# Optimization experiments

Measured on AMD Instinct MI355X. Metric: run time of the kernel, lower is better.

The kernel has to match this reference:

```python
import jax, jax.numpy as jnp
import numpy as np

B, T, C = 2, 2048, 1024
H, D = 16, 64          # n_heads, head_dim
E, K, HD = 8, 2, 1536  # num_experts, active_experts, expert hidden (int(1.5*C))
EPS = 1e-6


def setup_inputs() -> dict:
    key = jax.random.key(0)
    ks = jax.random.split(key, 13)
    s = 0.02
    return {
        "x": jax.random.normal(ks[0], (B, T, C), jnp.float32),
        "rope_cos": jax.random.uniform(ks[1], (T, D), jnp.float32),
        "rope_sin": jax.random.uniform(ks[2], (T, D), jnp.float32),
        "attn_norm_w": jnp.ones((C,), jnp.float32),
        "q_w": jax.random.normal(ks[3], (C, C), jnp.float32) * s,
        "k_w": jax.random.normal(ks[4], (C, C), jnp.float32) * s,
        "v_w": jax.random.normal(ks[5], (C, C), jnp.float32) * s,
        "o_w": jax.random.normal(ks[6], (C, C), jnp.float32) * s,
        "ffn_norm_w": jnp.ones((C,), jnp.float32),
        "router_w": jax.random.normal(ks[7], (E, C), jnp.float32) * s,
        "w1": jax.random.normal(ks[8], (E, HD, C), jnp.float32) * s,
        "w2": jax.random.normal(ks[9], (E, C, HD), jnp.float32) * s,
        "w3": jax.random.normal(ks[10], (E, HD, C), jnp.float32) * s,
    }


def rmsnorm(x, w):
    var = jnp.mean(x * x, axis=-1, keepdims=True)
    return w * x * jax.lax.rsqrt(var + EPS)


def apply_rope(x, cos, sin):
    # x: [B, T, H, D]; cos/sin: [T, D]
    cos = cos[None, :, None, :]
    sin = sin[None, :, None, :]
    d = x.shape[-1] // 2
    x1, x2 = x[..., :d], x[..., d:]
    rotated = jnp.concatenate([-x2, x1], axis=-1)
    return x * cos + rotated * sin


def reference(x, rope_cos, rope_sin, attn_norm_w, q_w, k_w, v_w, o_w,
              ffn_norm_w, router_w, w1, w2, w3):
    b, t, c = x.shape
    h = rmsnorm(x, attn_norm_w)
    q = (h @ q_w.T).reshape(b, t, H, D)
    k = (h @ k_w.T).reshape(b, t, H, D)
    v = (h @ v_w.T).reshape(b, t, H, D)
    q = apply_rope(q, rope_cos[:t], rope_sin[:t]).transpose(0, 2, 1, 3)  # [B,H,T,D]
    k = apply_rope(k, rope_cos[:t], rope_sin[:t]).transpose(0, 2, 1, 3)
    v = v.transpose(0, 2, 1, 3)
    scores = jnp.einsum('bhqd,bhkd->bhqk', q, k) / jnp.sqrt(jnp.asarray(D, q.dtype))
    causal = jnp.tril(jnp.ones((t, t), bool))
    scores = jnp.where(causal, scores, -jnp.inf)
    attn = jax.nn.softmax(scores, axis=-1)
    y = jnp.einsum('bhqk,bhkd->bhqd', attn, v)
    y = y.transpose(0, 2, 1, 3).reshape(b, t, c)
    x = x + y @ o_w.T

    # Sparse MoE (top-K routing, per-expert SwiGLU, weighted combine)
    hn = rmsnorm(x, ffn_norm_w)
    flat = hn.reshape(-1, c)                                # [N, C]
    logits = flat @ router_w.T                              # [N, E]
    wk, idx = jax.lax.top_k(logits, K)                      # [N, K]
    wk = jax.nn.softmax(wk, axis=-1)
    # combined per-expert gate: [N, E] (zero for unrouted experts)
    gate = jnp.sum((idx[..., None] == jnp.arange(E)) * wk[..., None], axis=1)
    out = jnp.zeros_like(flat)
    for e in range(E):
        g = jax.nn.silu(flat @ w1[e].T) * (flat @ w3[e].T)  # [N, HD]
        out = out + gate[:, e:e + 1] * (g @ w2[e].T)
    return x + out.reshape(b, t, c)
```

## Files before the change

### kernel.cpp

```cpp
#include <hip/hip_runtime.h>
#include <hip/hip_bf16.h>
#include <math.h>

#define Bq 2
#define Tq 2048
#define Cq 1024
#define Hq 16
#define Dq 64
#define Eq 8
#define HDq 1536
#define NTOK (Bq*Tq)

typedef unsigned short u16;
typedef unsigned int u32;
typedef _Float16 f16;
typedef __bf16 bf16x8 __attribute__((ext_vector_type(8)));
typedef _Float16 f16x8 __attribute__((ext_vector_type(8)));
typedef float f32x4v __attribute__((ext_vector_type(4)));

#define MB(x) ((size_t)(x) * 262144)

__device__ __forceinline__ float silu_f(float a) {
    return a / (1.0f + __expf(-a));
}
__device__ __forceinline__ u16 f2bf(float f) {
    union { float f; unsigned u; } a; a.f = f;
    unsigned r = a.u + 0x7fffu + ((a.u >> 16) & 1u);
    return (u16)(r >> 16);
}
__device__ __forceinline__ u16 f16bits(f16 h) {
    union { f16 f; u16 u; } a; a.f = h; return a.u;
}

__device__ __forceinline__ void stage16(const void* g, void* l) {
    __builtin_amdgcn_global_load_lds(
        (const __attribute__((address_space(1))) unsigned int*)g,
        (__attribute__((address_space(3))) unsigned int*)l, 16, 0, 0);
}

__global__ __launch_bounds__(256) void rmsnorm_split_k(const float* __restrict__ x,
                                                       const float* __restrict__ w,
                                                       u16* __restrict__ hh,
                                                       u16* __restrict__ hl) {
    int row = blockIdx.x;
    int tid = threadIdx.x;
    const float* xr = x + (size_t)row * Cq;
    float4 v = *(const float4*)(xr + tid * 4);
    float ss = v.x*v.x + v.y*v.y + v.z*v.z + v.w*v.w;
    #pragma unroll
    for (int off = 32; off; off >>= 1) ss += __shfl_xor(ss, off);
    __shared__ float red[4];
    if ((tid & 63) == 0) red[tid >> 6] = ss;
    __syncthreads();
    float tot = red[0] + red[1] + red[2] + red[3];
    float scale = rsqrtf(tot * (1.0f / (float)Cq) + 1e-6f);
    float4 wv = *(const float4*)(w + tid * 4);
    float o[4] = { v.x*wv.x*scale, v.y*wv.y*scale, v.z*wv.z*scale, v.w*wv.w*scale };
    ushort4 oh, ol;
    u16* ph = (u16*)&oh; u16* pl = (u16*)&ol;
    #pragma unroll
    for (int i = 0; i < 4; i++) {
        f16 hi = (f16)o[i]; f16 lo = (f16)(o[i] - (float)hi);
        ph[i] = f16bits(hi); pl[i] = f16bits(lo);
    }
    *(ushort4*)(hh + (size_t)row * Cq + tid * 4) = oh;
    *(ushort4*)(hl + (size_t)row * Cq + tid * 4) = ol;
}

__global__ __launch_bounds__(256) void rmsnorm2_k(const float* __restrict__ x,
                                                  const float* __restrict__ w,
                                                  float* __restrict__ hn,
                                                  u16* __restrict__ hnb) {
    int row = blockIdx.x;
    int tid = threadIdx.x;
    const float* xr = x + (size_t)row * Cq;
    float4 v = *(const float4*)(xr + tid * 4);
    float ss = v.x*v.x + v.y*v.y + v.z*v.z + v.w*v.w;
    #pragma unroll
    for (int off = 32; off; off >>= 1) ss += __shfl_xor(ss, off);
    __shared__ float red[4];
    if ((tid & 63) == 0) red[tid >> 6] = ss;
    __syncthreads();
    float tot = red[0] + red[1] + red[2] + red[3];
    float scale = rsqrtf(tot * (1.0f / (float)Cq) + 1e-6f);
    float4 wv = *(const float4*)(w + tid * 4);
    float4 o = make_float4(v.x*wv.x*scale, v.y*wv.y*scale, v.z*wv.z*scale, v.w*wv.w*scale);
    *(float4*)(hn + (size_t)row * Cq + tid * 4) = o;
    ushort4 ob = make_ushort4(f2bf(o.x), f2bf(o.y), f2bf(o.z), f2bf(o.w));
    *(ushort4*)(hnb + (size_t)row * Cq + tid * 4) = ob;
}

__global__ __launch_bounds__(256) void wconv_k(const float* __restrict__ w1,
                                               const float* __restrict__ w3,
                                               const float* __restrict__ w2,
                                               u16* __restrict__ w1b,
                                               u16* __restrict__ w3b,
                                               u16* __restrict__ w2b) {
    int a = blockIdx.y;
    const float* src = (a == 0) ? w1 : ((a == 1) ? w3 : w2);
    u16* dst = (a == 0) ? w1b : ((a == 1) ? w3b : w2b);
    size_t i = ((size_t)blockIdx.x * 256 + threadIdx.x) * 8;
    float4 f0 = *(const float4*)(src + i);
    float4 f1 = *(const float4*)(src + i + 4);
    ushort4 o0 = make_ushort4(f2bf(f0.x), f2bf(f0.y), f2bf(f0.z), f2bf(f0.w));
    ushort4 o1 = make_ushort4(f2bf(f1.x), f2bf(f1.y), f2bf(f1.z), f2bf(f1.w));
    *(ushort4*)(dst + i)     = o0;
    *(ushort4*)(dst + i + 4) = o1;
}

__global__ __launch_bounds__(256) void wsplit_k(const float* __restrict__ qw,
                                                const float* __restrict__ kw,
                                                const float* __restrict__ vw,
                                                const float* __restrict__ ow,
                                                u16* __restrict__ qhp, u16* __restrict__ qlp,
                                                u16* __restrict__ khp, u16* __restrict__ klp,
                                                u16* __restrict__ vhp, u16* __restrict__ vlp,
                                                u16* __restrict__ ohp, u16* __restrict__ olp) {
    int a = blockIdx.y;
    const float* src = (a == 0) ? qw : ((a == 1) ? kw : ((a == 2) ? vw : ow));
    u16* dh = (a == 0) ? qhp : ((a == 1) ? khp : ((a == 2) ? vhp : ohp));
    u16* dl = (a == 0) ? qlp : ((a == 1) ? klp : ((a == 2) ? vlp : olp));
    size_t i = ((size_t)blockIdx.x * 256 + threadIdx.x) * 8;
    float f[8];
    *(float4*)&f[0] = *(const float4*)(src + i);
    *(float4*)&f[4] = *(const float4*)(src + i + 4);
    u16 oh[8], ol[8];
    #pragma unroll
    for (int j = 0; j < 8; j++) {
        f16 hi = (f16)f[j]; f16 lo = (f16)(f[j] - (float)hi);
        oh[j] = f16bits(hi); ol[j] = f16bits(lo);
    }
    *(uint4*)(dh + i) = *(uint4*)oh;
    *(uint4*)(dl + i) = *(uint4*)ol;
}

__global__ __launch_bounds__(256, 3) void gemm_fused(const u16* __restrict__ Ahg,
                                                     const u16* __restrict__ Alg,
                                                     const float* __restrict__ Wq,
                                                     const float* __restrict__ Wk,
                                                     const float* __restrict__ Wv,
                                                     u16* __restrict__ qh_o,
                                                     u16* __restrict__ ql_o,
                                                     u16* __restrict__ kh_o,
                                                     u16* __restrict__ kl_o,
                                                     float* __restrict__ vf_o,
                                                     const float* __restrict__ cosb,
                                                     const float* __restrict__ sinb,
                                                     const float* __restrict__ aux,
                                                     float* __restrict__ outf,
                                                     int kind) {
    __shared__ u16 AhS[2][128*32], AlS[2][128*32], BhS[128*32], BlS[128*32];
    int tid = threadIdx.x;
    int wave = tid >> 6, lane = tid & 63;
    int wm = wave >> 1, wn = wave & 1;
    int bx = blockIdx.x, by = blockIdx.y;
    int proj, nx;
    const float* W;
    if (kind == 0) {
        proj = bx >> 3; nx = bx & 7;
        W = (proj == 0) ? Wq : ((proj == 1) ? Wk : Wv);
    } else {
        proj = 3; nx = bx; W = Wq;
    }

    int srow = tid >> 2, sch = (tid & 3) * 8;
    const u16* A0 = Ahg + (size_t)(by*128 + srow) * Cq + sch;
    const u16* A1 = A0 + (size_t)64 * Cq;
    const u16* L0 = Alg + (size_t)(by*128 + srow) * Cq + sch;
    const u16* L1 = L0 + (size_t)64 * Cq;
    const float* W0 = W + (size_t)(nx*128 + srow) * Cq + sch;
    const float* W1 = W0 + (size_t)64 * Cq;
    int lo0 = srow*32 + sch, lo1 = lo0 + 2048;

    f32x4v acc[4][4];
    #pragma unroll
    for (int i = 0; i < 4; i++)
        #pragma unroll
        for (int j = 0; j < 4; j++)
            #pragma unroll
            for (int r = 0; r < 4; r++) acc[i][j][r] = 0.0f;

    float wr0[8], wr1[8];
    stage16(A0, &AhS[0][lo0]);
    stage16(A1, &AhS[0][lo1]);
    stage16(L0, &AlS[0][lo0]);
    stage16(L1, &AlS[0][lo1]);
    *(float4*)&wr0[0] = *(const float4*)(W0);
    *(float4*)&wr0[4] = *(const float4*)(W0 + 4);
    *(float4*)&wr1[0] = *(const float4*)(W1);
    *(float4*)&wr1[4] = *(const float4*)(W1 + 4);

    int fr = lane & 15, fk = (lane >> 4) * 8;
    int cur = 0;
    for (int k0 = 0; k0 < Cq; k0 += 32, cur ^= 1) {
        __syncthreads();
        {
            f16x8 bh0, bl0, bh1, bl1;
            #pragma unroll
            for (int i = 0; i < 8; i++) {
                f16 h0 = (f16)wr0[i]; bh0[i] = h0; bl0[i] = (f16)(wr0[i] - (float)h0);
                f16 h1 = (f16)wr1[i]; bh1[i] = h1; bl1[i] = (f16)(wr1[i] - (float)h1);
            }
            *(f16x8*)(void*)&BhS[lo0] = bh0;
            *(f16x8*)(void*)&BlS[lo0] = bl0;
            *(f16x8*)(void*)&BhS[lo1] = bh1;
            *(f16x8*)(void*)&BlS[lo1] = bl1;
        }
        __syncthreads();
        int kn = k0 + 32;
        if (kn < Cq) {
            stage16(A0 + kn, &AhS[cur^1][lo0]);
            stage16(A1 + kn, &AhS[cur^1][lo1]);
            stage16(L0 + kn, &AlS[cur^1][lo0]);
            stage16(L1 + kn, &AlS[cur^1][lo1]);
            *(float4*)&wr0[0] = *(const float4*)(W0 + kn);
            *(float4*)&wr0[4] = *(const float4*)(W0 + kn + 4);
            *(float4*)&wr1[0] = *(const float4*)(W1 + kn);
            *(float4*)&wr1[4] = *(const float4*)(W1 + kn + 4);
        }
        f16x8 ah[4], al[4];
        #pragma unroll
        for (int mi = 0; mi < 4; mi++) {
            ah[mi] = *(const f16x8*)(const void*)&AhS[cur][(wm*64 + mi*16 + fr)*32 + fk];
            al[mi] = *(const f16x8*)(const void*)&AlS[cur][(wm*64 + mi*16 + fr)*32 + fk];
        }
        #pragma unroll
        for (int ni = 0; ni < 4; ni++) {
            f16x8 bhf = *(const f16x8*)(const void*)&BhS[(wn*64 + ni*16 + fr)*32 + fk];
            f16x8 blf = *(const f16x8*)(const void*)&BlS[(wn*64 + ni*16 + fr)*32 + fk];
            #pragma unroll
            for (int mi = 0; mi < 4; mi++) {
                acc[mi][ni] = __builtin_amdgcn_mfma_f32_16x16x32_f16(ah[mi], bhf, acc[mi][ni], 0, 0, 0);
                acc[mi][ni] = __builtin_amdgcn_mfma_f32_16x16x32_f16(ah[mi], blf, acc[mi][ni], 0, 0, 0);
                acc[mi][ni] = __builtin_amdgcn_mfma_f32_16x16x32_f16(al[mi], bhf, acc[mi][ni], 0, 0, 0);
            }
        }
    }

    int cr = (lane >> 4) * 4, cc = lane & 15;
    if (proj < 2) {
        u16* dh = (proj == 0) ? qh_o : kh_o;
        u16* dl = (proj == 0) ? ql_o : kl_o;
        float scale = (proj == 0) ? 0.125f : 1.0f;
        int hd = (nx * 2 + wn) * 64;
        #pragma unroll
        for (int mi = 0; mi < 4; mi++)
            #pragma unroll
            for (int r = 0; r < 4; r++) {
                int row = by*128 + wm*64 + mi*16 + cr + r;
                int t = row & (Tq - 1);
                #pragma unroll
                for (int ni = 0; ni < 2; ni++) {
                    int d0 = ni*16 + cc;
                    float a = acc[mi][ni][r];
                    float b = acc[mi][ni+2][r];
                    float c0 = cosb[t*Dq + d0],      s0 = sinb[t*Dq + d0];
                    float c1 = cosb[t*Dq + d0 + 32], s1 = sinb[t*Dq + d0 + 32];
                    float oa = (a * c0 - b * s0) * scale;
                    float ob = (b * c1 + a * s1) * scale;
                    size_t off = (size_t)row * Cq + hd + d0;
                    f16 ha = (f16)oa;
                    f16 hb = (f16)ob;
                    dh[off]      = f16bits(ha);
                    dl[off]      = f16bits((f16)(oa - (float)ha));
                    dh[off + 32] = f16bits(hb);
                    dl[off + 32] = f16bits((f16)(ob - (float)hb));
                }
            }
    } else if (proj == 2) {
        #pragma unroll
        for (int mi = 0; mi < 4; mi++)
            #pragma unroll
            for (int r = 0; r < 4; r++) {
                int row = by*128 + wm*64 + mi*16 + cr + r;
                #pragma unroll
                for (int ni = 0; ni < 4; ni++)
                    vf_o[(size_t)row * Cq + nx*128 + wn*64 + ni*16 + cc] = acc[mi][ni][r];
            }
    } else {
        #pragma unroll
        for (int mi = 0; mi < 4; mi++)
            #pragma unroll
            for (int r = 0; r < 4; r++) {
                int row = by*128 + wm*64 + mi*16 + cr + r;
                #pragma unroll
                for (int ni = 0; ni < 4; ni++) {
                    size_t off = (size_t)row * Cq + nx*128 + wn*64 + ni*16 + cc;
                    outf[off] = acc[mi][ni][r] + aux[off];
                }
            }
    }
}

__global__ __launch_bounds__(256, 2) void gemm_fused2(const u16* __restrict__ Ahg,
                                                      const u16* __restrict__ Alg,
                                                      const u16* __restrict__ Bh0,
                                                      const u16* __restrict__ Bl0,
                                                      const u16* __restrict__ Bh1,
                                                      const u16* __restrict__ Bl1,
                                                      const u16* __restrict__ Bh2,
                                                      const u16* __restrict__ Bl2,
                                                      u16* __restrict__ qh_o,
                                                      u16* __restrict__ ql_o,
                                                      u16* __restrict__ kh_o,
                                                      u16* __restrict__ kl_o,
                                                      float* __restrict__ vf_o,
                                                      const float* __restrict__ cosb,
                                                      const float* __restrict__ sinb,
                                                      const float* __restrict__ aux,
                                                      float* __restrict__ outf,
                                                      int kind) {
    __shared__ u16 AhS[2][128*32], AlS[2][128*32], BhS[2][128*32], BlS[2][128*32];
    int tid = threadIdx.x;
    int wave = tid >> 6, lane = tid & 63;
    int wm = wave >> 1, wn = wave & 1;
    int bx = blockIdx.x, by = blockIdx.y;
    int proj, nx;
    const u16 *Bh, *Bl;
    if (kind == 0) {
        proj = bx >> 3; nx = bx & 7;
        Bh = (proj == 0) ? Bh0 : ((proj == 1) ? Bh1 : Bh2);
        Bl = (proj == 0) ? Bl0 : ((proj == 1) ? Bl1 : Bl2);
    } else {
        proj = 3; nx = bx; Bh = Bh0; Bl = Bl0;
    }

    int srow = tid >> 2, sch = (tid & 3) * 8;
    const u16* A0 = Ahg + (size_t)(by*128 + srow) * Cq + sch;
    const u16* A1 = A0 + (size_t)64 * Cq;
    const u16* L0 = Alg + (size_t)(by*128 + srow) * Cq + sch;
    const u16* L1 = L0 + (size_t)64 * Cq;
    const u16* H0 = Bh + (size_t)(nx*128 + srow) * Cq + sch;
    const u16* H1 = H0 + (size_t)64 * Cq;
    const u16* G0 = Bl + (size_t)(nx*128 + srow) * Cq + sch;
    const u16* G1 = G0 + (size_t)64 * Cq;
    int lo0 = srow*32 + sch, lo1 = lo0 + 2048;

    f32x4v acc[4][4];
    #pragma unroll
    for (int i = 0; i < 4; i++)
        #pragma unroll
        for (int j = 0; j < 4; j++)
            #pragma unroll
            for (int r = 0; r < 4; r++) acc[i][j][r] = 0.0f;

    stage16(A0, &AhS[0][lo0]); stage16(A1, &AhS[0][lo1]);
    stage16(L0, &AlS[0][lo0]); stage16(L1, &AlS[0][lo1]);
    stage16(H0, &BhS[0][lo0]); stage16(H1, &BhS[0][lo1]);
    stage16(G0, &BlS[0][lo0]); stage16(G1, &BlS[0][lo1]);

    int fr = lane & 15, fk = (lane >> 4) * 8;
    int cur = 0;
    for (int k0 = 0; k0 < Cq; k0 += 32, cur ^= 1) {
        __syncthreads();
        int kn = k0 + 32;
        if (kn < Cq) {
            stage16(A0 + kn, &AhS[cur^1][lo0]); stage16(A1 + kn, &AhS[cur^1][lo1]);
            stage16(L0 + kn, &AlS[cur^1][lo0]); stage16(L1 + kn, &AlS[cur^1][lo1]);
            stage16(H0 + kn, &BhS[cur^1][lo0]); stage16(H1 + kn, &BhS[cur^1][lo1]);
            stage16(G0 + kn, &BlS[cur^1][lo0]); stage16(G1 + kn, &BlS[cur^1][lo1]);
        }
        f16x8 ah[4], al[4];
        #pragma unroll
        for (int mi = 0; mi < 4; mi++) {
            ah[mi] = *(const f16x8*)(const void*)&AhS[cur][(wm*64 + mi*16 + fr)*32 + fk];
            al[mi] = *(const f16x8*)(const void*)&AlS[cur][(wm*64 + mi*16 + fr)*32 + fk];
        }
        #pragma unroll
        for (int ni = 0; ni < 4; ni++) {
            f16x8 bhf = *(const f16x8*)(const void*)&BhS[cur][(wn*64 + ni*16 + fr)*32 + fk];
            f16x8 blf = *(const f16x8*)(const void*)&BlS[cur][(wn*64 + ni*16 + fr)*32 + fk];
            #pragma unroll
            for (int mi = 0; mi < 4; mi++) {
                acc[mi][ni] = __builtin_amdgcn_mfma_f32_16x16x32_f16(ah[mi], bhf, acc[mi][ni], 0, 0, 0);
                acc[mi][ni] = __builtin_amdgcn_mfma_f32_16x16x32_f16(ah[mi], blf, acc[mi][ni], 0, 0, 0);
                acc[mi][ni] = __builtin_amdgcn_mfma_f32_16x16x32_f16(al[mi], bhf, acc[mi][ni], 0, 0, 0);
            }
        }
    }

    int cr = (lane >> 4) * 4, cc = lane & 15;
    if (proj < 2) {
        u16* dh = (proj == 0) ? qh_o : kh_o;
        u16* dl = (proj == 0) ? ql_o : kl_o;
        float scale = (proj == 0) ? 0.125f : 1.0f;
        int hd = (nx * 2 + wn) * 64;
        #pragma unroll
        for (int mi = 0; mi < 4; mi++)
            #pragma unroll
            for (int r = 0; r < 4; r++) {
                int row = by*128 + wm*64 + mi*16 + cr + r;
                int t = row & (Tq - 1);
                #pragma unroll
                for (int ni = 0; ni < 2; ni++) {
                    int d0 = ni*16 + cc;
                    float a = acc[mi][ni][r];
                    float b = acc[mi][ni+2][r];
                    float c0 = cosb[t*Dq + d0],      s0 = sinb[t*Dq + d0];
                    float c1 = cosb[t*Dq + d0 + 32], s1 = sinb[t*Dq + d0 + 32];
                    float oa = (a * c0 - b * s0) * scale;
                    float ob = (b * c1 + a * s1) * scale;
                    size_t off = (size_t)row * Cq + hd + d0;
                    f16 ha = (f16)oa;
                    f16 hb = (f16)ob;
                    dh[off]      = f16bits(ha);
                    dl[off]      = f16bits((f16)(oa - (float)ha));
                    dh[off + 32] = f16bits(hb);
                    dl[off + 32] = f16bits((f16)(ob - (float)hb));
                }
            }
    } else if (proj == 2) {
        #pragma unroll
        for (int mi = 0; mi < 4; mi++)
            #pragma unroll
            for (int r = 0; r < 4; r++) {
                int row = by*128 + wm*64 + mi*16 + cr + r;
                #pragma unroll
                for (int ni = 0; ni < 4; ni++)
                    vf_o[(size_t)row * Cq + nx*128 + wn*64 + ni*16 + cc] = acc[mi][ni][r];
            }
    } else {
        #pragma unroll
        for (int mi = 0; mi < 4; mi++)
            #pragma unroll
            for (int r = 0; r < 4; r++) {
                int row = by*128 + wm*64 + mi*16 + cr + r;
                #pragma unroll
                for (int ni = 0; ni < 4; ni++) {
                    size_t off = (size_t)row * Cq + nx*128 + wn*64 + ni*16 + cc;
                    outf[off] = acc[mi][ni][r] + aux[off];
                }
            }
    }
}

__global__ __launch_bounds__(256) void vtrans_k(const float* __restrict__ v,
                                                u16* __restrict__ vth,
                                                u16* __restrict__ vtl) {
    __shared__ u16 Th[64 * 72];
    __shared__ u16 Tl[64 * 72];
    int tc = blockIdx.x;
    int bh = blockIdx.y;
    int b = bh >> 4, h = bh & 15;
    int tid = threadIdx.x;
    int tr = tid >> 2;
    int dc = (tid & 3) * 16;
    size_t gin = ((size_t)(b * Tq + tc * 64 + tr)) * Cq + h * Dq + dc;
    #pragma unroll
    for (int i = 0; i < 16; i += 4) {
        float4 f = *(const float4*)(v + gin + i);
        float fv[4] = {f.x, f.y, f.z, f.w};
        #pragma unroll
        for (int j = 0; j < 4; j++) {
            f16 hi = (f16)fv[j];
            f16 lo = (f16)(fv[j] - (float)hi);
            Th[(dc + i + j) * 72 + tr] = f16bits(hi);
            Tl[(dc + i + j) * 72 + tr] = f16bits(lo);
        }
    }
    __syncthreads();
    int dr = tid >> 2;
    int cc = (tid & 3) * 16;
    size_t gout = ((size_t)(bh * 64 + dr)) * Tq + tc * 64 + cc;
    *(uint4*)(vth + gout)     = *(uint4*)(Th + dr * 72 + cc);
    *(uint4*)(vth + gout + 8) = *(uint4*)(Th + dr * 72 + cc + 8);
    *(uint4*)(vtl + gout)     = *(uint4*)(Tl + dr * 72 + cc);
    *(uint4*)(vtl + gout + 8) = *(uint4*)(Tl + dr * 72 + cc + 8);
}

#define AST 72
__global__ __launch_bounds__(256, 3) void attn_f16(const u16* __restrict__ qh_g,
                                                   const u16* __restrict__ ql_g,
                                                   const u16* __restrict__ kh_g,
                                                   const u16* __restrict__ kl_g,
                                                   const u16* __restrict__ vth_g,
                                                   const u16* __restrict__ vtl_g,
                                                   u16* __restrict__ yh_g,
                                                   u16* __restrict__ yl_g) {
    __shared__ u16 Kh[64*AST], Kl[64*AST];
    __shared__ u16 Vh[64*AST], Vl[64*AST];

    int id = blockIdx.x;
    int bh = id & 31;
    int qt = 31 - (id >> 5);
    int b = bh >> 4, h = bh & 15;
    int tid = threadIdx.x;
    int wv = tid >> 6, lane = tid & 63;
    int fr = lane & 15, fg = lane >> 4;
    int sr = tid >> 2, sc = (tid & 3) * 16;

    int idx0 = fr + ((fg & 1) << 5);
    int idx1 = idx0 + 16;
    int hiw = fg >> 1;

    uint4 rkh0, rkh1, rkl0, rkl1, rvh0, rvh1, rvl0, rvl1;
    auto ldkv = [&](int kt) {
        size_t kg = ((size_t)(b * Tq + kt * 64 + sr)) * Cq + h * Dq + sc;
        size_t vg = ((size_t)(bh * 64 + sr)) * Tq + kt * 64 + sc;
        rkh0 = *(const uint4*)(kh_g + kg);  rkh1 = *(const uint4*)(kh_g + kg + 8);
        rkl0 = *(const uint4*)(kl_g + kg);  rkl1 = *(const uint4*)(kl_g + kg + 8);
        rvh0 = *(const uint4*)(vth_g + vg); rvh1 = *(const uint4*)(vth_g + vg + 8);
        rvl0 = *(const uint4*)(vtl_g + vg); rvl1 = *(const uint4*)(vtl_g + vg + 8);
    };

    size_t qg = ((size_t)(b * Tq + qt * 64 + wv * 16 + fr)) * Cq + h * Dq + fg * 8;
    f16x8 aqh0 = *(const f16x8*)(const void*)(qh_g + qg);
    f16x8 aqh1 = *(const f16x8*)(const void*)(qh_g + qg + 32);
    f16x8 aql0 = *(const f16x8*)(const void*)(ql_g + qg);
    f16x8 aql1 = *(const f16x8*)(const void*)(ql_g + qg + 32);
    ldkv(0);

    f32x4v acc_o[4];
    float m_i = -1e30f, l_i = 0.0f;
    #pragma unroll
    for (int i = 0; i < 4; i++)
        #pragma unroll
        for (int r = 0; r < 4; r++) acc_o[i][r] = 0.0f;

    for (int kt = 0; kt <= qt; kt++) {
        __syncthreads();
        *(uint4*)(Kh + sr*AST + sc)     = rkh0;
        *(uint4*)(Kh + sr*AST + sc + 8) = rkh1;
        *(uint4*)(Kl + sr*AST + sc)     = rkl0;
        *(uint4*)(Kl + sr*AST + sc + 8) = rkl1;
        *(uint4*)(Vh + sr*AST + sc)     = rvh0;
        *(uint4*)(Vh + sr*AST + sc + 8) = rvh1;
        *(uint4*)(Vl + sr*AST + sc)     = rvl0;
        *(uint4*)(Vl + sr*AST + sc + 8) = rvl1;
        __syncthreads();
        if (kt < qt) ldkv(kt + 1);

        f32x4v s[4];
        __builtin_amdgcn_s_setprio(1);
        #pragma unroll
        for (int ni = 0; ni < 4; ni++) {
            int boff = (ni * 16 + fr) * AST + fg * 8;
            f16x8 kh0 = *(const f16x8*)(const void*)(Kh + boff);
            f16x8 kh1 = *(const f16x8*)(const void*)(Kh + boff + 32);
            f16x8 kl0 = *(const f16x8*)(const void*)(Kl + boff);
            f16x8 kl1 = *(const f16x8*)(const void*)(Kl + boff + 32);
            f32x4v t;
            #pragma unroll
            for (int r = 0; r < 4; r++) t[r] = 0.0f;
            t = __builtin_amdgcn_mfma_f32_16x16x32_f16(kh0, aqh0, t, 0, 0, 0);
            t = __builtin_amdgcn_mfma_f32_16x16x32_f16(kh1, aqh1, t, 0, 0, 0);
            t = __builtin_amdgcn_mfma_f32_16x16x32_f16(kl0, aqh0, t, 0, 0, 0);
            t = __builtin_amdgcn_mfma_f32_16x16x32_f16(kl1, aqh1, t, 0, 0, 0);
            t = __builtin_amdgcn_mfma_f32_16x16x32_f16(kh0, aql0, t, 0, 0, 0);
            t = __builtin_amdgcn_mfma_f32_16x16x32_f16(kh1, aql1, t, 0, 0, 0);
            s[ni] = t;
        }
        __builtin_amdgcn_s_setprio(0);

        if (kt == qt) {
            int qloc = wv * 16 + fr;
            #pragma unroll
            for (int ni = 0; ni < 4; ni++) {
                #pragma unroll
                for (int r = 0; r < 4; r++) {
                    if (ni * 16 + fg * 4 + r > qloc) s[ni][r] = -1e30f;
                }
            }
        }

        float mx = s[0][0];
        #pragma unroll
        for (int ni = 0; ni < 4; ni++)
            #pragma unroll
            for (int r = 0; r < 4; r++) mx = fmaxf(mx, s[ni][r]);
        mx = fmaxf(mx, __shfl_xor(mx, 16));
        mx = fmaxf(mx, __shfl_xor(mx, 32));
        float mn = fmaxf(m_i, mx);
        float p[4][4];
        float rs = 0.0f;
        #pragma unroll
        for (int ni = 0; ni < 4; ni++)
            #pragma unroll
            for (int r = 0; r < 4; r++) {
                p[ni][r] = __expf(s[ni][r] - mn);
                rs += p[ni][r];
            }
        rs += __shfl_xor(rs, 16);
        rs += __shfl_xor(rs, 32);
        float alpha = __expf(m_i - mn);
        l_i = l_i * alpha + rs;
        m_i = mn;

        #pragma unroll
        for (int r = 0; r < 4; r++) {
            float ar = __shfl(alpha, 20 * fg + r);
            #pragma unroll
            for (int ni = 0; ni < 4; ni++) acc_o[ni][r] *= ar;
        }

        u32 wh[8], wl[8];
        #pragma unroll
        for (int ni = 0; ni < 4; ni++) {
            #pragma unroll
            for (int pr = 0; pr < 2; pr++) {
                float pa = p[ni][pr*2], pb = p[ni][pr*2 + 1];
                f16 ha = (f16)pa, hb = (f16)pb;
                wh[ni*2 + pr] = (u32)f16bits(ha) | ((u32)f16bits(hb) << 16);
                f16 la = (f16)(pa - (float)ha), lb = (f16)(pb - (float)hb);
                wl[ni*2 + pr] = (u32)f16bits(la) | ((u32)f16bits(lb) << 16);
            }
        }

        union { u32 u[4]; f16x8 v; } fh0, fh1, fl0, fl1;
        {
            u32 a, c;
            a = __shfl((int)wh[0], idx0); c = __shfl((int)wh[2], idx0);
            fh0.u[0] = hiw ? c : a;
            a = __shfl((int)wh[1], idx0); c = __shfl((int)wh[3], idx0);
            fh0.u[1] = hiw ? c : a;
            a = __shfl((int)wh[0], idx1); c = __shfl((int)wh[2], idx1);
            fh0.u[2] = hiw ? c : a;
            a = __shfl((int)wh[1], idx1); c = __shfl((int)wh[3], idx1);
            fh0.u[3] = hiw ? c : a;
            a = __shfl((int)wh[4], idx0); c = __shfl((int)wh[6], idx0);
            fh1.u[0] = hiw ? c : a;
            a = __shfl((int)wh[5], idx0); c = __shfl((int)wh[7], idx0);
            fh1.u[1] = hiw ? c : a;
            a = __shfl((int)wh[4], idx1); c = __shfl((int)wh[6], idx1);
            fh1.u[2] = hiw ? c : a;
            a = __shfl((int)wh[5], idx1); c = __shfl((int)wh[7], idx1);
            fh1.u[3] = hiw ? c : a;
            a = __shfl((int)wl[0], idx0); c = __shfl((int)wl[2], idx0);
            fl0.u[0] = hiw ? c : a;
            a = __shfl((int)wl[1], idx0); c = __shfl((int)wl[3], idx0);
            fl0.u[1] = hiw ? c : a;
            a = __shfl((int)wl[0], idx1); c = __shfl((int)wl[2], idx1);
            fl0.u[2] = hiw ? c : a;
            a = __shfl((int)wl[1], idx1); c = __shfl((int)wl[3], idx1);
            fl0.u[3] = hiw ? c : a;
            a = __shfl((int)wl[4], idx0); c = __shfl((int)wl[6], idx0);
            fl1.u[0] = hiw ? c : a;
            a = __shfl((int)wl[5], idx0); c = __shfl((int)wl[7], idx0);
            fl1.u[1] = hiw ? c : a;
            a = __shfl((int)wl[4], idx1); c = __shfl((int)wl[6], idx1);
            fl1.u[2] = hiw ? c : a;
            a = __shfl((int)wl[5], idx1); c = __shfl((int)wl[7], idx1);
            fl1.u[3] = hiw ? c : a;
        }

        __builtin_amdgcn_s_setprio(1);
        #pragma unroll
        for (int ni = 0; ni < 4; ni++) {
            int boff = (ni * 16 + fr) * AST + fg * 8;
            f16x8 vh0 = *(const f16x8*)(const void*)(Vh + boff);
            f16x8 vh1 = *(const f16x8*)(const void*)(Vh + boff + 32);
            f16x8 vl0 = *(const f16x8*)(const void*)(Vl + boff);
            f16x8 vl1 = *(const f16x8*)(const void*)(Vl + boff + 32);
            f32x4v t = acc_o[ni];
            t = __builtin_amdgcn_mfma_f32_16x16x32_f16(fh0.v, vh0, t, 0, 0, 0);
            t = __builtin_amdgcn_mfma_f32_16x16x32_f16(fh1.v, vh1, t, 0, 0, 0);
            t = __builtin_amdgcn_mfma_f32_16x16x32_f16(fh0.v, vl0, t, 0, 0, 0);
            t = __builtin_amdgcn_mfma_f32_16x16x32_f16(fh1.v, vl1, t, 0, 0, 0);
            t = __builtin_amdgcn_mfma_f32_16x16x32_f16(fl0.v, vh0, t, 0, 0, 0);
            t = __builtin_amdgcn_mfma_f32_16x16x32_f16(fl1.v, vh1, t, 0, 0, 0);
            acc_o[ni] = t;
        }
        __builtin_amdgcn_s_setprio(0);
    }

    #pragma unroll
    for (int r = 0; r < 4; r++) {
        float lq = __shfl(l_i, 20 * fg + r);
        float inv = 1.0f / lq;
        int row = qt * 64 + wv * 16 + fg * 4 + r;
        size_t base = ((size_t)(b * Tq + row)) * Cq + h * Dq + fr;
        #pragma unroll
        for (int ni = 0; ni < 4; ni++) {
            float yv = acc_o[ni][r] * inv;
            f16 hi = (f16)yv;
            f16 lo = (f16)(yv - (float)hi);
            yh_g[base + ni * 16] = f16bits(hi);
            yl_g[base + ni * 16] = f16bits(lo);
        }
    }
}

__global__ void zero_k(int* cnt) {
    if (threadIdx.x < Eq) cnt[threadIdx.x] = 0;
}

__global__ __launch_bounds__(64) void router_k(const float* __restrict__ hn,
                                               const float* __restrict__ rw,
                                               int* __restrict__ cnt,
                                               int* __restrict__ idxl,
                                               float* __restrict__ gvl) {
    int tkn = blockIdx.x;
    int lane = threadIdx.x;
    float acc[Eq] = {};
    for (int it = 0; it < Cq / 64; it++) {
        float hv = hn[(size_t)tkn * Cq + it * 64 + lane];
        #pragma unroll
        for (int e = 0; e < Eq; e++)
            acc[e] = fmaf(hv, rw[e * Cq + it * 64 + lane], acc[e]);
    }
    #pragma unroll
    for (int e = 0; e < Eq; e++) {
        #pragma unroll
        for (int off = 32; off; off >>= 1) acc[e] += __shfl_xor(acc[e], off);
    }
    int i0 = 0;
    #pragma unroll
    for (int e = 1; e < Eq; e++) if (acc[e] > acc[i0]) i0 = e;
    int i1 = (i0 == 0) ? 1 : 0;
    #pragma unroll
    for (int e = 0; e < Eq; e++)
        if (e != i0 && acc[e] > acc[i1]) i1 = e;
    float p1 = __expf(acc[i1] - acc[i0]);
    float g0 = 1.0f / (1.0f + p1);
    float g1 = p1 / (1.0f + p1);
    if (lane == 0) {
        int p0 = atomicAdd(&cnt[i0], 1);
        idxl[i0 * NTOK + p0] = tkn;
        gvl[i0 * NTOK + p0] = g0;
        int p1i = atomicAdd(&cnt[i1], 1);
        idxl[i1 * NTOK + p1i] = tkn;
        gvl[i1 * NTOK + p1i] = g1;
    }
}

__global__ void setup_k(const int* __restrict__ cnt, int* __restrict__ seg,
                        int* __restrict__ texp, int* __restrict__ ttot) {
    if (threadIdx.x == 0) {
        int base = 0;
        for (int e = 0; e < Eq; e++) {
            seg[e] = base * 128;
            int t = (cnt[e] + 127) >> 7;
            for (int i = 0; i < t; i++) texp[base + i] = e;
            base += t;
        }
        *ttot = base;
    }
}

__global__ __launch_bounds__(256, 2) void moe_w13b(const u16* __restrict__ hnb,
                                                   const u16* __restrict__ w1b,
                                                   const u16* __restrict__ w3b,
                                                   u16* __restrict__ gbuf,
                                                   const int* __restrict__ cnt,
                                                   const int* __restrict__ seg,
                                                   const int* __restrict__ texp,
                                                   const int* __restrict__ ttot,
                                                   const int* __restrict__ idxl) {
    int by = blockIdx.y;
    if (by >= *ttot) return;
    int e = texp[by];
    const u16* w1e = w1b + (size_t)e * HDq * Cq;
    const u16* w3e = w3b + (size_t)e * HDq * Cq;
    int cnte = cnt[e], sege = seg[e];
    const int* idxe = idxl + e * NTOK;

    __shared__ u16 As[2][128*32], B1S[2][128*32], B3S[2][128*32];
    int tid = threadIdx.x;
    int wave = tid >> 6, lane = tid & 63;
    int wm = wave >> 1, wn = wave & 1;
    int bx = blockIdx.x;
    int srow = tid >> 2, sch = (tid & 3) * 8;

    int r0 = by*128 + srow, r1 = r0 + 64;
    int li0 = r0 - sege, li1 = r1 - sege;
    int tok0 = idxe[li0 < cnte ? li0 : 0];
    int tok1 = idxe[li1 < cnte ? li1 : 0];
    const u16* A0 = hnb + (size_t)tok0 * Cq + sch;
    const u16* A1 = hnb + (size_t)tok1 * Cq + sch;
    const u16* W10 = w1e + (size_t)(bx*128 + srow) * Cq + sch;
    const u16* W11 = W10 + (size_t)64 * Cq;
    const u16* W30 = w3e + (size_t)(bx*128 + srow) * Cq + sch;
    const u16* W31 = W30 + (size_t)64 * Cq;
    int lo0 = srow*32 + sch, lo1 = lo0 + 2048;

    f32x4v acc1[4][4], acc3[4][4];
    #pragma unroll
    for (int i = 0; i < 4; i++)
        #pragma unroll
        for (int j = 0; j < 4; j++)
            #pragma unroll
            for (int r = 0; r < 4; r++) { acc1[i][j][r] = 0.0f; acc3[i][j][r] = 0.0f; }

    stage16(A0,  &As[0][lo0]);  stage16(A1,  &As[0][lo1]);
    stage16(W10, &B1S[0][lo0]); stage16(W11, &B1S[0][lo1]);
    stage16(W30, &B3S[0][lo0]); stage16(W31, &B3S[0][lo1]);

    int fr = lane & 15, fk = (lane >> 4) * 8;
    int cur = 0;
    for (int k0 = 0; k0 < Cq; k0 += 32, cur ^= 1) {
        __syncthreads();
        int kn = k0 + 32;
        if (kn < Cq) {
            stage16(A0 + kn,  &As[cur^1][lo0]);  stage16(A1 + kn,  &As[cur^1][lo1]);
            stage16(W10 + kn, &B1S[cur^1][lo0]); stage16(W11 + kn, &B1S[cur^1][lo1]);
            stage16(W30 + kn, &B3S[cur^1][lo0]); stage16(W31 + kn, &B3S[cur^1][lo1]);
        }
        bf16x8 af[4];
        #pragma unroll
        for (int mi = 0; mi < 4; mi++)
            af[mi] = *(const bf16x8*)&As[cur][(wm*64 + mi*16 + fr) * 32 + fk];
        #pragma unroll
        for (int ni = 0; ni < 4; ni++) {
            bf16x8 b1f = *(const bf16x8*)&B1S[cur][(wn*64 + ni*16 + fr) * 32 + fk];
            bf16x8 b3f = *(const bf16x8*)&B3S[cur][(wn*64 + ni*16 + fr) * 32 + fk];
            #pragma unroll
            for (int mi = 0; mi < 4; mi++) {
                acc1[mi][ni] = __builtin_amdgcn_mfma_f32_16x16x32_bf16(af[mi], b1f, acc1[mi][ni], 0, 0, 0);
                acc3[mi][ni] = __builtin_amdgcn_mfma_f32_16x16x32_bf16(af[mi], b3f, acc3[mi][ni], 0, 0, 0);
            }
        }
    }

    int cr = (lane >> 4) * 4, cc = lane & 15;
    #pragma unroll
    for (int mi = 0; mi < 4; mi++)
        #pragma unroll
        for (int ni = 0; ni < 4; ni++)
            #pragma unroll
            for (int r = 0; r < 4; r++) {
                int row = by*128 + wm*64 + mi*16 + cr + r;
                int col = bx*128 + wn*64 + ni*16 + cc;
                gbuf[(size_t)row * HDq + col] = f2bf(silu_f(acc1[mi][ni][r]) * acc3[mi][ni][r]);
            }
}

__global__ __launch_bounds__(256, 3) void moe_w2b_k(const u16* __restrict__ gbuf,
                                                    const u16* __restrict__ w2b,
                                                    float* __restrict__ out,
                                                    const int* __restrict__ cnt,
                                                    const int* __restrict__ seg,
                                                    const int* __restrict__ texp,
                                                    const int* __restrict__ ttot,
                                                    const int* __restrict__ idxl,
                                                    const float* __restrict__ gvl) {
    int by = blockIdx.y;
    if (by >= *ttot) return;
    int e = texp[by];
    const u16* w2e = w2b + (size_t)e * Cq * HDq;
// ... 188 lines not shown
                                                 const int* __restrict__ seg,
                                                 const int* __restrict__ texp,
                                                 const int* __restrict__ ttot,
                                                 const int* __restrict__ idxl,
                                                 const float* __restrict__ gvl) {
    int by = blockIdx.y;
    if (by >= *ttot) return;
    int e = texp[by];
    const float* w2e = w2 + (size_t)e * Cq * HDq;
    int cnte = cnt[e], sege = seg[e];
    const int* idxe = idxl + e * NTOK;
    const float* gve = gvl + e * NTOK;

    __shared__ u16 As[2][128*32], Bs[128*32];
    int tid = threadIdx.x;
    int wave = tid >> 6, lane = tid & 63;
    int wm = wave >> 1, wn = wave & 1;
    int bx = blockIdx.x;
    int srow = tid >> 2, sch = (tid & 3) * 8;

    const u16* A0 = gbuf + (size_t)(by*128 + srow) * HDq + sch;
    const u16* A1 = A0 + (size_t)64 * HDq;
    const float* W0 = w2e + (size_t)(bx*128 + srow) * HDq + sch;
    const float* W1 = W0 + (size_t)64 * HDq;
    int lo0 = srow*32 + sch, lo1 = lo0 + 2048;

    f32x4v acc[4][4];
    #pragma unroll
    for (int i = 0; i < 4; i++)
        #pragma unroll
        for (int j = 0; j < 4; j++)
            #pragma unroll
            for (int r = 0; r < 4; r++) acc[i][j][r] = 0.0f;

    float xa[8], xb[8];
    stage16(A0, &As[0][lo0]);
    stage16(A1, &As[0][lo1]);
    *(float4*)&xa[0] = *(const float4*)(W0);
    *(float4*)&xa[4] = *(const float4*)(W0 + 4);
    *(float4*)&xb[0] = *(const float4*)(W1);
    *(float4*)&xb[4] = *(const float4*)(W1 + 4);

    int fr = lane & 15, fk = (lane >> 4) * 8;
    int cur = 0;
    for (int k0 = 0; k0 < HDq; k0 += 32, cur ^= 1) {
        __syncthreads();
        {
            u16 ta[8], tb[8];
            #pragma unroll
            for (int i = 0; i < 8; i++) { ta[i] = f2bf(xa[i]); tb[i] = f2bf(xb[i]); }
            *(uint4*)&Bs[lo0] = *(uint4*)ta;
            *(uint4*)&Bs[lo1] = *(uint4*)tb;
        }
        __syncthreads();
        int kn = k0 + 32;
        if (kn < HDq) {
            stage16(A0 + kn, &As[cur^1][lo0]);
            stage16(A1 + kn, &As[cur^1][lo1]);
            *(float4*)&xa[0] = *(const float4*)(W0 + kn);
            *(float4*)&xa[4] = *(const float4*)(W0 + kn + 4);
            *(float4*)&xb[0] = *(const float4*)(W1 + kn);
            *(float4*)&xb[4] = *(const float4*)(W1 + kn + 4);
        }
        bf16x8 af[4];
        #pragma unroll
        for (int mi = 0; mi < 4; mi++)
            af[mi] = *(const bf16x8*)&As[cur][(wm*64 + mi*16 + fr) * 32 + fk];
        #pragma unroll
        for (int ni = 0; ni < 4; ni++) {
            bf16x8 bf_ = *(const bf16x8*)&Bs[(wn*64 + ni*16 + fr) * 32 + fk];
            #pragma unroll
            for (int mi = 0; mi < 4; mi++)
                acc[mi][ni] = __builtin_amdgcn_mfma_f32_16x16x32_bf16(af[mi], bf_, acc[mi][ni], 0, 0, 0);
        }
    }

    int cr = (lane >> 4) * 4, cc = lane & 15;
    #pragma unroll
    for (int mi = 0; mi < 4; mi++)
        #pragma unroll
        for (int r = 0; r < 4; r++) {
            int row = by*128 + wm*64 + mi*16 + cr + r;
            int local = row - sege;
            if (local < cnte) {
                int token = idxe[local];
                float g = gve[local];
                #pragma unroll
                for (int ni = 0; ni < 4; ni++) {
                    int col = bx*128 + wn*64 + ni*16 + cc;
                    atomicAdd(&out[(size_t)token * Cq + col], g * acc[mi][ni][r]);
                }
            }
        }
}

extern "C" void kernel_launch(void* const* d_in, const int* in_sizes, int n_in,
                              void* d_out, int out_size, void* d_ws, size_t ws_size,
                              hipStream_t stream) {
    (void)in_sizes; (void)n_in; (void)out_size;

    const float* x     = (const float*)d_in[0];
    const float* ropec = (const float*)d_in[1];
    const float* ropes = (const float*)d_in[2];
    const float* anw   = (const float*)d_in[3];
    const float* q_w   = (const float*)d_in[4];
    const float* k_w   = (const float*)d_in[5];
    const float* v_w   = (const float*)d_in[6];
    const float* o_w   = (const float*)d_in[7];
    const float* fnw   = (const float*)d_in[8];
    const float* rtw   = (const float*)d_in[9];
    const float* w1    = (const float*)d_in[10];
    const float* w2    = (const float*)d_in[11];
    const float* w3    = (const float*)d_in[12];
    float* out = (float*)d_out;

    float* ws = (float*)d_ws;
    u16* hh = (u16*)(ws + MB(0));
    u16* hl = (u16*)(ws + MB(8));
    float* vf = ws + MB(16);
    u16* qh = (u16*)(ws + MB(32));
    u16* ql = (u16*)(ws + MB(40));
    u16* kh = (u16*)(ws + MB(48));
    u16* kl = (u16*)(ws + MB(56));
    u16* vth = (u16*)(ws + MB(0));
    u16* vtl = (u16*)(ws + MB(8));
    u16* yh  = (u16*)(ws + MB(16));
    u16* yl  = (u16*)(ws + MB(24));
    u16* gbuf = (u16*)(ws + MB(0));
    float* hn = ws + MB(32);
    u16* hnb  = (u16*)(ws + MB(48));
    int* cntp = (int*)(ws + MB(56));
    int* segp = cntp + 8;
    int* texp = cntp + 16;
    int* ttot = cntp + 96;
    int* idxl = cntp + 256;
    float* gvl = (float*)(cntp + 256 + Eq*NTOK);
    u16* w1b = (u16*)(ws + MB(64));
    u16* w3b = (u16*)(ws + MB(88));
    u16* w2b = (u16*)(ws + MB(112));
    u16* wqh = (u16*)(ws + MB(136));
    u16* wql = (u16*)(ws + MB(138));
    u16* wkh = (u16*)(ws + MB(140));
    u16* wkl = (u16*)(ws + MB(142));
    u16* wvh = (u16*)(ws + MB(144));
    u16* wvl = (u16*)(ws + MB(146));
    u16* woh = (u16*)(ws + MB(148));
    u16* wol = (u16*)(ws + MB(150));

    const int M = NTOK;
    const bool pre  = ws_size >= ((size_t)136 << 20);
    const bool pre2 = ws_size >= ((size_t)152 << 20);

    if (pre)
        hipLaunchKernelGGL(wconv_k, dim3(6144, 3), dim3(256), 0, stream,
                           w1, w3, w2, w1b, w3b, w2b);
    if (pre2)
        hipLaunchKernelGGL(wsplit_k, dim3(512, 4), dim3(256), 0, stream,
                           q_w, k_w, v_w, o_w,
                           wqh, wql, wkh, wkl, wvh, wvl, woh, wol);

    hipLaunchKernelGGL(rmsnorm_split_k, dim3(M), dim3(256), 0, stream, x, anw, hh, hl);

    if (pre2)
        hipLaunchKernelGGL(gemm_fused2, dim3(24, M/128), dim3(256), 0, stream,
                           hh, hl, wqh, wql, wkh, wkl, wvh, wvl,
                           qh, ql, kh, kl, vf,
                           ropec, ropes, (const float*)nullptr, (float*)nullptr, 0);
    else
        hipLaunchKernelGGL(gemm_fused, dim3(24, M/128), dim3(256), 0, stream,
                           hh, hl, q_w, k_w, v_w, qh, ql, kh, kl, vf,
                           ropec, ropes, (const float*)nullptr, (float*)nullptr, 0);

    hipLaunchKernelGGL(vtrans_k, dim3(32, 32), dim3(256), 0, stream, vf, vth, vtl);

    hipLaunchKernelGGL(attn_f16, dim3(1024), dim3(256), 0, stream,
                       qh, ql, kh, kl, vth, vtl, yh, yl);

    if (pre2)
        hipLaunchKernelGGL(gemm_fused2, dim3(8, M/128), dim3(256), 0, stream,
                           yh, yl, woh, wol,
                           (const u16*)nullptr, (const u16*)nullptr,
                           (const u16*)nullptr, (const u16*)nullptr,
                           (u16*)nullptr, (u16*)nullptr, (u16*)nullptr, (u16*)nullptr,
                           (float*)nullptr, ropec, ropes, x, out, 1);
    else
        hipLaunchKernelGGL(gemm_fused, dim3(8, M/128), dim3(256), 0, stream,
                           yh, yl, o_w, (const float*)nullptr, (const float*)nullptr,
                           (u16*)nullptr, (u16*)nullptr, (u16*)nullptr, (u16*)nullptr,
                           (float*)nullptr, ropec, ropes, x, out, 1);

    hipLaunchKernelGGL(rmsnorm2_k, dim3(M), dim3(256), 0, stream, out, fnw, hn, hnb);

    hipLaunchKernelGGL(zero_k, dim3(1), dim3(64), 0, stream, cntp);
    hipLaunchKernelGGL(router_k, dim3(M), dim3(64), 0, stream, hn, rtw, cntp, idxl, gvl);
    hipLaunchKernelGGL(setup_k, dim3(1), dim3(64), 0, stream, cntp, segp, texp, ttot);

    if (pre) {
        hipLaunchKernelGGL(moe_w13b, dim3(HDq/128, 72), dim3(256), 0, stream,
                           hnb, w1b, w3b, gbuf, cntp, segp, texp, ttot, idxl);
        hipLaunchKernelGGL(moe_w2b_k, dim3(Cq/128, 72), dim3(256), 0, stream,
                           gbuf, w2b, out, cntp, segp, texp, ttot, idxl, gvl);
    } else {
        hipLaunchKernelGGL(moe_w13, dim3(HDq/128, 72), dim3(256), 0, stream,
                           hnb, w1, w3, gbuf, cntp, segp, texp, ttot, idxl);
        hipLaunchKernelGGL(moe_w2, dim3(Cq/128, 72), dim3(256), 0, stream,
                           gbuf, w2, out, cntp, segp, texp, ttot, idxl, gvl);
    }
}
```

Measured before the change: 718.1 us.

## Load GEMM B fragments directly from global, merge weight-prep and zero kernels

The gemm_fused2 kernel stops staging the weight (B) tiles through shared memory and instead loads each wave's B fragments straight from global memory into registers. This halves LDS use and lets launch bounds rise to 3 blocks per CU. The two weight-conversion kernels are merged into one launch, and the counter zeroing is folded into rmsnorm2_k, cutting two launches. The risk is uncoalesced or duplicated global B loads across waves, without the double buffering that previously hid their latency. Zeroing the counters inside rmsnorm2_k is only safe because the router kernel that reads them runs in a later launch.

```diff
diff --git a/kernel.cpp b/kernel.cpp
--- a/kernel.cpp
+++ b/kernel.cpp
@@ -70,9 +70,11 @@
 __global__ __launch_bounds__(256) void rmsnorm2_k(const float* __restrict__ x,
                                                   const float* __restrict__ w,
                                                   float* __restrict__ hn,
-                                                  u16* __restrict__ hnb) {
+                                                  u16* __restrict__ hnb,
+                                                  int* __restrict__ cnt) {
     int row = blockIdx.x;
     int tid = threadIdx.x;
+    if (row == 0 && tid < Eq) cnt[tid] = 0;
     const float* xr = x + (size_t)row * Cq;
     float4 v = *(const float4*)(xr + tid * 4);
     float ss = v.x*v.x + v.y*v.y + v.z*v.z + v.w*v.w;
@@ -90,48 +92,51 @@
     *(ushort4*)(hnb + (size_t)row * Cq + tid * 4) = ob;
 }
 
-__global__ __launch_bounds__(256) void wconv_k(const float* __restrict__ w1,
+__global__ __launch_bounds__(256) void wprep_k(const float* __restrict__ w1,
                                                const float* __restrict__ w3,
                                                const float* __restrict__ w2,
+                                               const float* __restrict__ qw,
+                                               const float* __restrict__ kw,
+                                               const float* __restrict__ vw,
+                                               const float* __restrict__ ow,
                                                u16* __restrict__ w1b,
                                                u16* __restrict__ w3b,
-                                               u16* __restrict__ w2b) {
-    int a = blockIdx.y;
-    const float* src = (a == 0) ? w1 : ((a == 1) ? w3 : w2);
-    u16* dst = (a == 0) ? w1b : ((a == 1) ? w3b : w2b);
-    size_t i = ((size_t)blockIdx.x * 256 + threadIdx.x) * 8;
-    float4 f0 = *(const float4*)(src + i);
-    float4 f1 = *(const float4*)(src + i + 4);
-    ushort4 o0 = make_ushort4(f2bf(f0.x), f2bf(f0.y), f2bf(f0.z), f2bf(f0.w));
-    ushort4 o1 = make_ushort4(f2bf(f1.x), f2bf(f1.y), f2bf(f1.z), f2bf(f1.w));
-    *(ushort4*)(dst + i)     = o0;
-    *(ushort4*)(dst + i + 4) = o1;
-}
-
-__global__ __launch_bounds__(256) void wsplit_k(const float* __restrict__ qw,
-                                                const float* __restrict__ kw,
-                                                const float* __restrict__ vw,
-                                                const float* __restrict__ ow,
-                                                u16* __restrict__ qhp, u16* __restrict__ qlp,
-                                                u16* __restrict__ khp, u16* __restrict__ klp,
-                                                u16* __restrict__ vhp, u16* __restrict__ vlp,
-                                                u16* __restrict__ ohp, u16* __restrict__ olp) {
-    int a = blockIdx.y;
-    const float* src = (a == 0) ? qw : ((a == 1) ? kw : ((a == 2) ? vw : ow));
-    u16* dh = (a == 0) ? qhp : ((a == 1) ? khp : ((a == 2) ? vhp : ohp));
-    u16* dl = (a == 0) ? qlp : ((a == 1) ? klp : ((a == 2) ? vlp : olp));
-    size_t i = ((size_t)blockIdx.x * 256 + threadIdx.x) * 8;
-    float f[8];
-    *(float4*)&f[0] = *(const float4*)(src + i);
-    *(float4*)&f[4] = *(const float4*)(src + i + 4);
-    u16 oh[8], ol[8];
-    #pragma unroll
-    for (int j = 0; j < 8; j++) {
-        f16 hi = (f16)f[j]; f16 lo = (f16)(f[j] - (float)hi);
-        oh[j] = f16bits(hi); ol[j] = f16bits(lo);
-    }
-    *(uint4*)(dh + i) = *(uint4*)oh;
-    *(uint4*)(dl + i) = *(uint4*)ol;
+                                               u16* __restrict__ w2b,
+                                               u16* __restrict__ qhp, u16* __restrict__ qlp,
+                                               u16* __restrict__ khp, u16* __restrict__ klp,
+                                               u16* __restrict__ vhp, u16* __restrict__ vlp,
+                                               u16* __restrict__ ohp, u16* __restrict__ olp) {
+    int yg = blockIdx.y;
+    if (yg < 3) {
+        const float* src = (yg == 0) ? w1 : ((yg == 1) ? w3 : w2);
+        u16* dst = (yg == 0) ? w1b : ((yg == 1) ? w3b : w2b);
+        size_t i = ((size_t)blockIdx.x * 256 + threadIdx.x) * 8;
+        float4 f0 = *(const float4*)(src + i);
+        float4 f1 = *(const float4*)(src + i + 4);
+        ushort4 o0 = make_ushort4(f2bf(f0.x), f2bf(f0.y), f2bf(f0.z), f2bf(f0.w));
+        ushort4 o1 = make_ushort4(f2bf(f1.x), f2bf(f1.y), f2bf(f1.z), f2bf(f1.w));
+        *(ushort4*)(dst + i)     = o0;
+        *(ushort4*)(dst + i + 4) = o1;
+    } else {
+        int x = blockIdx.x;
+        if (x >= 2048) return;
+        int a = x >> 9;
+        const float* src = (a == 0) ? qw : ((a == 1) ? kw : ((a == 2) ? vw : ow));
+        u16* dh = (a == 0) ? qhp : ((a == 1) ? khp : ((a == 2) ? vhp : ohp));
+        u16* dl = (a == 0) ? qlp : ((a == 1) ? klp : ((a == 2) ? vlp : olp));
+        size_t i = ((size_t)(x & 511) * 256 + threadIdx.x) * 8;
+        float f[8];
+        *(float4*)&f[0] = *(const float4*)(src + i);
+        *(float4*)&f[4] = *(const float4*)(src + i + 4);
+        u16 oh[8], ol[8];
+        #pragma unroll
+        for (int j = 0; j < 8; j++) {
+            f16 hi = (f16)f[j]; f16 lo = (f16)(f[j] - (float)hi);
+            oh[j] = f16bits(hi); ol[j] = f16bits(lo);
+        }
+        *(uint4*)(dh + i) = *(uint4*)oh;
+        *(uint4*)(dl + i) = *(uint4*)ol;
+    }
 }
 
 __global__ __launch_bounds__(256, 3) void gemm_fused(const u16* __restrict__ Ahg,
@@ -292,7 +297,7 @@
     }
 }
 
-__global__ __launch_bounds__(256, 2) void gemm_fused2(const u16* __restrict__ Ahg,
+__global__ __launch_bounds__(256, 3) void gemm_fused2(const u16* __restrict__ Ahg,
                                                       const u16* __restrict__ Alg,
                                                       const u16* __restrict__ Bh0,
                                                       const u16* __restrict__ Bl0,
@@ -310,7 +315,7 @@
                                                       const float* __restrict__ aux,
                                                       float* __restrict__ outf,
                                                       int kind) {
-    __shared__ u16 AhS[2][128*32], AlS[2][128*32], BhS[2][128*32], BlS[2][128*32];
+    __shared__ u16 AhS[2][128*32], AlS[2][128*32];
     int tid = threadIdx.x;
     int wave = tid >> 6, lane = tid & 63;
     int wm = wave >> 1, wn = wave & 1;
@@ -330,11 +335,13 @@
     const u16* A1 = A0 + (size_t)64 * Cq;
     const u16* L0 = Alg + (size_t)(by*128 + srow) * Cq + sch;
     const u16* L1 = L0 + (size_t)64 * Cq;
-    const u16* H0 = Bh + (size_t)(nx*128 + srow) * Cq + sch;
-    const u16* H1 = H0 + (size_t)64 * Cq;
-    const u16* G0 = Bl + (size_t)(nx*128 + srow) * Cq + sch;
-    const u16* G1 = G0 + (size_t)64 * Cq;
     int lo0 = srow*32 + sch, lo1 = lo0 + 2048;
+
+    int fr = lane & 15, fk = (lane >> 4) * 8;
+    size_t bbase[4];
+    #pragma unroll
+    for (int ni = 0; ni < 4; ni++)
+        bbase[ni] = (size_t)(nx*128 + wn*64 + ni*16 + fr) * Cq + fk;
 
     f32x4v acc[4][4];
     #pragma unroll
@@ -346,10 +353,7 @@
 
     stage16(A0, &AhS[0][lo0]); stage16(A1, &AhS[0][lo1]);
     stage16(L0, &AlS[0][lo0]); stage16(L1, &AlS[0][lo1]);
-    stage16(H0, &BhS[0][lo0]); stage16(H1, &BhS[0][lo1]);
-    stage16(G0, &BlS[0][lo0]); stage16(G1, &BlS[0][lo1]);
-
-    int fr = lane & 15, fk = (lane >> 4) * 8;
+
     int cur = 0;
     for (int k0 = 0; k0 < Cq; k0 += 32, cur ^= 1) {
         __syncthreads();
@@ -357,8 +361,12 @@
         if (kn < Cq) {
             stage16(A0 + kn, &AhS[cur^1][lo0]); stage16(A1 + kn, &AhS[cur^1][lo1]);
             stage16(L0 + kn, &AlS[cur^1][lo0]); stage16(L1 + kn, &AlS[cur^1][lo1]);
-            stage16(H0 + kn, &BhS[cur^1][lo0]); stage16(H1 + kn, &BhS[cur^1][lo1]);
-            stage16(G0 + kn, &BlS[cur^1][lo0]); stage16(G1 + kn, &BlS[cur^1][lo1]);
+        }
+        f16x8 bh[4], bl[4];
+        #pragma unroll
+        for (int ni = 0; ni < 4; ni++) {
+            bh[ni] = *(const f16x8*)(const void*)(Bh + bbase[ni] + k0);
+            bl[ni] = *(const f16x8*)(const void*)(Bl + bbase[ni] + k0);
         }
         f16x8 ah[4], al[4];
         #pragma unroll
@@ -368,13 +376,11 @@
         }
         #pragma unroll
         for (int ni = 0; ni < 4; ni++) {
-            f16x8 bhf = *(const f16x8*)(const void*)&BhS[cur][(wn*64 + ni*16 + fr)*32 + fk];
-            f16x8 blf = *(const f16x8*)(const void*)&BlS[cur][(wn*64 + ni*16 + fr)*32 + fk];
             #pragma unroll
             for (int mi = 0; mi < 4; mi++) {
-                acc[mi][ni] = __builtin_amdgcn_mfma_f32_16x16x32_f16(ah[mi], bhf, acc[mi][ni], 0, 0, 0);
-                acc[mi][ni] = __builtin_amdgcn_mfma_f32_16x16x32_f16(ah[mi], blf, acc[mi][ni], 0, 0, 0);
-                acc[mi][ni] = __builtin_amdgcn_mfma_f32_16x16x32_f16(al[mi], bhf, acc[mi][ni], 0, 0, 0);
+                acc[mi][ni] = __builtin_amdgcn_mfma_f32_16x16x32_f16(ah[mi], bh[ni], acc[mi][ni], 0, 0, 0);
+                acc[mi][ni] = __builtin_amdgcn_mfma_f32_16x16x32_f16(ah[mi], bl[ni], acc[mi][ni], 0, 0, 0);
+                acc[mi][ni] = __builtin_amdgcn_mfma_f32_16x16x32_f16(al[mi], bh[ni], acc[mi][ni], 0, 0, 0);
             }
         }
     }
@@ -680,10 +686,6 @@
     }
 }
 
-__global__ void zero_k(int* cnt) {
-    if (threadIdx.x < Eq) cnt[threadIdx.x] = 0;
-}
-
 __global__ __launch_bounds__(64) void router_k(const float* __restrict__ hn,
                                                const float* __restrict__ rw,
                                                int* __restrict__ cnt,
@@ -1178,11 +1180,9 @@
     const bool pre2 = ws_size >= ((size_t)152 << 20);
 
     if (pre)
-        hipLaunchKernelGGL(wconv_k, dim3(6144, 3), dim3(256), 0, stream,
-                           w1, w3, w2, w1b, w3b, w2b);
-    if (pre2)
-        hipLaunchKernelGGL(wsplit_k, dim3(512, 4), dim3(256), 0, stream,
-                           q_w, k_w, v_w, o_w,
+        hipLaunchKernelGGL(wprep_k, dim3(6144, pre2 ? 4 : 3), dim3(256), 0, stream,
+                           w1, w3, w2, q_w, k_w, v_w, o_w,
+                           w1b, w3b, w2b,
                            wqh, wql, wkh, wkl, wvh, wvl, woh, wol);
 
     hipLaunchKernelGGL(rmsnorm_split_k, dim3(M), dim3(256), 0, stream, x, anw, hh, hl);
@@ -1215,9 +1215,8 @@
                            (u16*)nullptr, (u16*)nullptr, (u16*)nullptr, (u16*)nullptr,
                            (float*)nullptr, ropec, ropes, x, out, 1);
 
-    hipLaunchKernelGGL(rmsnorm2_k, dim3(M), dim3(256), 0, stream, out, fnw, hn, hnb);
-
-    hipLaunchKernelGGL(zero_k, dim3(1), dim3(64), 0, stream, cntp);
+    hipLaunchKernelGGL(rmsnorm2_k, dim3(M), dim3(256), 0, stream, out, fnw, hn, hnb, cntp);
+
     hipLaunchKernelGGL(router_k, dim3(M), dim3(64), 0, stream, hn, rtw, cntp, idxl, gvl);
     hipLaunchKernelGGL(setup_k, dim3(1), dim3(64), 0, stream, cntp, segp, texp, ttot);
 
```

Measured after the change: 762.9 us. 6.2% more time.
